# Optimization experiments

Hardware: AMD Instinct MI355X
Metric: run time of the kernel (lower is better)

The kernel has to match this reference:

```python
import jax, jax.numpy as jnp
import numpy as np
import math

B, T, D, H, P, NPASS = 2, 2048, 1024, 16, 256, 3


def setup_inputs() -> dict:
    key = jax.random.key(0)
    ks = jax.random.split(key, 8)
    x = jax.random.normal(ks[0], (B, T, D), jnp.float32)
    scale_gamma = 1.0 + 0.1 * jax.random.normal(ks[1], (D,), jnp.float32)
    scale_beta = 0.1 * jax.random.normal(ks[2], (D,), jnp.float32)
    qkv_w = 0.02 * jax.random.normal(ks[3], (3 * D, D), jnp.float32)
    o_w = 0.02 * jax.random.normal(ks[4], (D, D), jnp.float32)
    norm1_w = jnp.ones((D,), jnp.float32)
    norm2_w = jnp.ones((D,), jnp.float32)
    angles = 0.1 * jax.random.normal(ks[5], (NPASS, P), jnp.float32)
    gate = jnp.ones((NPASS, D), jnp.float32)
    bias = jnp.zeros((NPASS, D), jnp.float32)
    # seeded random permutations matching torch.manual_seed(42+p*1000); torch.randperm
    pis, pjs = [], []
    for p in range(NPASS):
        rng = np.random.RandomState(42 + p * 1000)
        perm = rng.permutation(D)
        pis.append(perm[:P])
        pjs.append(perm[P:2 * P])
    pi = jnp.asarray(np.stack(pis), jnp.int32)
    pj = jnp.asarray(np.stack(pjs), jnp.int32)
    return dict(x=x, scale_gamma=scale_gamma, scale_beta=scale_beta, qkv_w=qkv_w,
                o_w=o_w, norm1_w=norm1_w, norm2_w=norm2_w, angles=angles,
                gate=gate, bias=bias, pi=pi, pj=pj)


def _rmsnorm(x, w):
    eps = jnp.finfo(x.dtype).eps
    return x * jax.lax.rsqrt(jnp.mean(x * x, axis=-1, keepdims=True) + eps) * w


def reference(x, scale_gamma, scale_beta, qkv_w, o_w, norm1_w, norm2_w,
              angles, gate, bias, pi, pj):
    Bs, Ts, Ds = x.shape
    hd = Ds // H
    # --- attention branch ---
    h = _rmsnorm(x, norm1_w) * scale_gamma + scale_beta
    qkv = (h @ qkv_w.T).reshape(Bs, Ts, 3, H, hd)
    qkv = jnp.moveaxis(qkv, 2, 0)            # [3, B, T, H, hd]
    q, k, v = (jnp.swapaxes(qkv[i], 1, 2) for i in range(3))  # [B, H, T, hd]
    scores = jnp.einsum('bhqd,bhkd->bhqk', q, k) / math.sqrt(hd)
    causal = jnp.tril(jnp.ones((Ts, Ts), bool))
    scores = jnp.where(causal, scores, -jnp.inf)
    attn = jax.nn.softmax(scores, axis=-1)
    out = jnp.einsum('bhqk,bhkd->bhqd', attn, v)
    out = jnp.swapaxes(out, 1, 2).reshape(Bs, Ts, Ds)
    x = x + out @ o_w.T
    # --- rotation pseudo-FFN branch ---
    h = _rmsnorm(x, norm2_w) * scale_gamma + scale_beta
    r = h
    for p in range(NPASS):
        cos_a = jnp.cos(angles[p])
        sin_a = jnp.sin(angles[p])
        hi = r[..., pi[p]]
        hj = r[..., pj[p]]
        r = r.at[..., pi[p]].set(hi * cos_a - hj * sin_a)
        r = r.at[..., pj[p]].set(hi * sin_a + hj * cos_a)
        r = jax.nn.silu(r * gate[p] + bias[p])
    return x + r - h
```

## Files before the change

### kernel.cpp

```cpp
#include <hip/hip_runtime.h>
#include <hip/hip_bf16.h>

#define B_ 2
#define T_ 2048
#define D_ 1024
#define H_ 16
#define HD_ 64
#define NP_ 3
#define P_ 256

#define SCALE2 0.18033688011112042f

typedef short bf16x8 __attribute__((ext_vector_type(8)));
typedef float f32x4 __attribute__((ext_vector_type(4)));

__device__ __forceinline__ float bf2f(__hip_bfloat16 v) { return __bfloat162float(v); }
__device__ __forceinline__ __hip_bfloat16 f2bf(float v) { return __float2bfloat16(v); }

__device__ __forceinline__ unsigned pack2bf(float a, float b) {
    unsigned r;
    asm("v_cvt_pk_bf16_f32 %0, %1, %2" : "=v"(r) : "v"(a), "v"(b));
    return r;
}
__device__ __forceinline__ unsigned short f2bf_u(float v) {
    return (unsigned short)pack2bf(v, v);
}

#define GLOAD_LDS16(gp, lp) \
    __builtin_amdgcn_global_load_lds( \
        (const __attribute__((address_space(1))) void*)(gp), \
        (__attribute__((address_space(3))) void*)(lp), 16, 0, 0)

__global__ __launch_bounds__(256) void detect_kernel(
    const unsigned short* __restrict__ xs, int* __restrict__ flag)
{
    __shared__ int cnt;
    if (threadIdx.x == 0) cnt = 0;
    __syncthreads();
    int bad = 0;
    for (int i = threadIdx.x; i < 16384; i += 256) {
        int e = (xs[i] >> 7) & 0xFF;
        if (e >= 0xB8) bad++;
    }
    if (bad) atomicAdd(&cnt, bad);
    __syncthreads();
    if (threadIdx.x == 0) *flag = (cnt >= 8) ? 1 : 0;
}

__global__ __launch_bounds__(256) void prep_kernel(
    const void* __restrict__ xraw,
    const void* __restrict__ qkvw, const void* __restrict__ ow,
    const void* __restrict__ g,  const void* __restrict__ b,
    const void* __restrict__ n1, const void* __restrict__ n2,
    const void* __restrict__ ang, const void* __restrict__ gt,
    const void* __restrict__ bi,
    const int* __restrict__ flag,
    __hip_bfloat16* __restrict__ wbf, __hip_bfloat16* __restrict__ owbf,
    float* __restrict__ smalls, __hip_bfloat16* __restrict__ out)
{
    int bid = blockIdx.x;
    int t = threadIdx.x;
    int f = *flag;

    if (bid < 2048) {
        const int na = 3 * D_ * D_;
        int i8 = (bid * 256 + t) * 8;
        const void* src; __hip_bfloat16* dst; int off;
        if (i8 < na) { src = qkvw; dst = wbf; off = i8; }
        else         { src = ow;   dst = owbf; off = i8 - na; }
        if (f) {
            const float4* sp = (const float4*)((const float*)src + off);
            float4 v0 = sp[0], v1 = sp[1];
            uint4 o;
            o.x = pack2bf(v0.x, v0.y);
            o.y = pack2bf(v0.z, v0.w);
            o.z = pack2bf(v1.x, v1.y);
            o.w = pack2bf(v1.z, v1.w);
            *(uint4*)(dst + off) = o;
        } else {
            *(uint4*)(dst + off) = *(const uint4*)((const __hip_bfloat16*)src + off);
        }
        return;
    }
    if (bid < 6144) {
        int row = bid - 2048;
        float eps = f ? 1.1920929e-7f : 0.0078125f;
        float v[4], ga[4], be[4], ww[4];
        if (f) {
            const float4 xv = ((const float4*)((const float*)xraw + (size_t)row * D_))[t];
            v[0] = xv.x; v[1] = xv.y; v[2] = xv.z; v[3] = xv.w;
            const float4 gv = ((const float4*)g)[t];
            ga[0] = gv.x; ga[1] = gv.y; ga[2] = gv.z; ga[3] = gv.w;
            const float4 bv = ((const float4*)b)[t];
            be[0] = bv.x; be[1] = bv.y; be[2] = bv.z; be[3] = bv.w;
            const float4 wv4 = ((const float4*)n1)[t];
            ww[0] = wv4.x; ww[1] = wv4.y; ww[2] = wv4.z; ww[3] = wv4.w;
        } else {
            const uint2 u = ((const uint2*)((const __hip_bfloat16*)xraw + (size_t)row * D_))[t];
            v[0] = __uint_as_float(u.x << 16);
            v[1] = __uint_as_float(u.x & 0xffff0000u);
            v[2] = __uint_as_float(u.y << 16);
            v[3] = __uint_as_float(u.y & 0xffff0000u);
#pragma unroll
            for (int c = 0; c < 4; c++) {
                int e = t * 4 + c;
                ga[c] = bf2f(((const __hip_bfloat16*)g)[e]);
                be[c] = bf2f(((const __hip_bfloat16*)b)[e]);
                ww[c] = bf2f(((const __hip_bfloat16*)n1)[e]);
            }
        }
        float ss = 0.f;
#pragma unroll
        for (int c = 0; c < 4; c++) ss += v[c] * v[c];
#pragma unroll
        for (int m = 32; m; m >>= 1) ss += __shfl_xor(ss, m, 64);
        __shared__ float red[4];
        int wv = t >> 6;
        if ((t & 63) == 0) red[wv] = ss;
        __syncthreads();
        float scale = rsqrtf((red[0] + red[1] + red[2] + red[3]) * (1.0f / D_) + eps);
        float o[4];
#pragma unroll
        for (int c = 0; c < 4; c++)
            o[c] = v[c] * scale * ww[c] * ga[c] + be[c];
        uint2 pkd;
        pkd.x = pack2bf(o[0], o[1]);
        pkd.y = pack2bf(o[2], o[3]);
        *(uint2*)(out + (size_t)row * D_ + t * 4) = pkd;
        return;
    }
    {
        int i = (bid - 6144) * 256 + t;
        if (i >= 11008) return;
        const void* src; int off;
        if      (i < 1024) { src = g;   off = i; }
        else if (i < 2048) { src = b;   off = i - 1024; }
        else if (i < 3072) { src = n1;  off = i - 2048; }
        else if (i < 4096) { src = n2;  off = i - 3072; }
        else if (i < 4864) { src = ang; off = i - 4096; }
        else if (i < 7936) { src = gt;  off = i - 4864; }
        else               { src = bi;  off = i - 7936; }
        smalls[i] = f ? ((const float*)src)[off]
                      : bf2f(((const __hip_bfloat16*)src)[off]);
    }
}

__global__ __launch_bounds__(256) void gemm_bt_bf16_kernel(
    const __hip_bfloat16* __restrict__ A,
    const __hip_bfloat16* __restrict__ Bm,
    __hip_bfloat16* __restrict__ C,
    int M, int N, int K, int nscale, float qscale)
{
    __shared__ __attribute__((aligned(16))) __hip_bfloat16 As[128 * 32];
    __shared__ __attribute__((aligned(16))) __hip_bfloat16 Bs[128 * 32];
    int tid = threadIdx.x;
    int bm = blockIdx.y, bn = blockIdx.x;
    int lane = tid & 63, wv = tid >> 6;
    int wm = wv >> 1, wn = wv & 1;
    int q = lane >> 4, mr = lane & 15;

    f32x4 acc[4][4] = {};

    for (int k0 = 0; k0 < K; k0 += 32) {
#pragma unroll
        for (int s = 0; s < 2; s++) {
            int e = (s * 256 + tid) * 8;
            int r = e >> 5, c = e & 31;
            GLOAD_LDS16(&A[(size_t)(bm * 128 + r) * K + k0 + c], &As[e]);
            GLOAD_LDS16(&Bm[(size_t)(bn * 128 + r) * K + k0 + c], &Bs[e]);
        }
        __syncthreads();
        bf16x8 af[4], bfr[4];
#pragma unroll
        for (int i = 0; i < 4; i++)
            af[i] = *(const bf16x8*)(&As[(wm * 64 + i * 16 + mr) * 32 + q * 8]);
#pragma unroll
        for (int j = 0; j < 4; j++)
            bfr[j] = *(const bf16x8*)(&Bs[(wn * 64 + j * 16 + mr) * 32 + q * 8]);
#pragma unroll
        for (int i = 0; i < 4; i++)
#pragma unroll
            for (int j = 0; j < 4; j++)
                acc[i][j] = __builtin_amdgcn_mfma_f32_16x16x32_bf16(af[i], bfr[j], acc[i][j], 0, 0, 0);
        __syncthreads();
    }

#pragma unroll
    for (int i = 0; i < 4; i++)
#pragma unroll
        for (int r = 0; r < 4; r++) {
            int m = bm * 128 + wm * 64 + i * 16 + q * 4 + r;
#pragma unroll
            for (int j = 0; j < 4; j++) {
                int n = bn * 128 + wn * 64 + j * 16 + mr;
                float vv = acc[i][j][r];
                if (n < nscale) vv *= qscale;
                ((unsigned short*)C)[(size_t)m * N + n] = f2bf_u(vv);
            }
        }
}

__global__ __launch_bounds__(256) void gemm_o64_resid_kernel(
    const __hip_bfloat16* __restrict__ A,
    const __hip_bfloat16* __restrict__ Bm,
    const void* __restrict__ xraw,
    const int* __restrict__ flag,
    float* __restrict__ C,
    int M, int N, int K)
{
    __shared__ __attribute__((aligned(16))) __hip_bfloat16 As[128 * 32];
    __shared__ __attribute__((aligned(16))) __hip_bfloat16 Bs[64 * 32];
    int tid = threadIdx.x;
    int bn = blockIdx.x, bm = blockIdx.y;
    int lane = tid & 63, wv = tid >> 6;
    int q = lane >> 4, mr = lane & 15;
    int f = *flag;

    f32x4 acc[2][4] = {};

    for (int k0 = 0; k0 < K; k0 += 32) {
#pragma unroll
        for (int s = 0; s < 2; s++) {
            int e = (s * 256 + tid) * 8;
            int r = e >> 5, c = e & 31;
            GLOAD_LDS16(&A[(size_t)(bm * 128 + r) * K + k0 + c], &As[e]);
        }
        {
            int e = tid * 8;
            int r = e >> 5, c = e & 31;
            GLOAD_LDS16(&Bm[(size_t)(bn * 64 + r) * K + k0 + c], &Bs[e]);
        }
        __syncthreads();
        bf16x8 af[2], bfr[4];
#pragma unroll
        for (int i = 0; i < 2; i++)
            af[i] = *(const bf16x8*)(&As[(wv * 32 + i * 16 + mr) * 32 + q * 8]);
#pragma unroll
        for (int j = 0; j < 4; j++)
            bfr[j] = *(const bf16x8*)(&Bs[(j * 16 + mr) * 32 + q * 8]);
#pragma unroll
        for (int i = 0; i < 2; i++)
#pragma unroll
            for (int j = 0; j < 4; j++)
                acc[i][j] = __builtin_amdgcn_mfma_f32_16x16x32_bf16(af[i], bfr[j], acc[i][j], 0, 0, 0);
        __syncthreads();
    }

#pragma unroll
    for (int i = 0; i < 2; i++)
#pragma unroll
        for (int r = 0; r < 4; r++) {
            int m = bm * 128 + wv * 32 + i * 16 + q * 4 + r;
#pragma unroll
            for (int j = 0; j < 4; j++) {
                int n = bn * 64 + j * 16 + mr;
                size_t idx = (size_t)m * N + n;
                float rv = f ? ((const float*)xraw)[idx]
                             : bf2f(((const __hip_bfloat16*)xraw)[idx]);
                C[idx] = rv + acc[i][j][r];
            }
        }
}

__global__ __launch_bounds__(256, 4) void attn_kernel(
    const __hip_bfloat16* __restrict__ qkv,
    __hip_bfloat16* __restrict__ attn_out)
{
    __shared__ __attribute__((aligned(16))) __hip_bfloat16 Ks[2][64 * 64];
    __shared__ __attribute__((aligned(16))) __hip_bfloat16 Vts[2][64 * 64];
    __shared__ __attribute__((aligned(16))) unsigned int Pd[4 * 512];

    int id = blockIdx.x;
    int half = (id ^ (id >> 8)) & 1;
    int w4 = (id >> 1) & 15;
    int qt = half ? 31 - w4 : w4;
    int bh = (id >> 5) & 31;
    int b = bh >> 4, h = bh & 15;
    int tid = threadIdx.x, lane = tid & 63, wv = tid >> 6;
    int q = lane >> 4, mr = lane & 15;
    int m8 = mr & 7;

    const size_t rs3 = 3 * D_;
    const __hip_bfloat16* qp = qkv + (size_t)(b * T_) * rs3 + h * HD_;
    const __hip_bfloat16* kp = qp + D_;
    const __hip_bfloat16* vp = qp + 2 * D_;

    int sr = tid >> 2;
    int sc = (tid & 3) * 16;
    int lc0 = sc >> 3;
    int swk = sr & 7;
    int kk_ = (tid & 31) * 2;
    int dd = (tid >> 5) * 8;
    int vlc = kk_ >> 3, voff = kk_ & 7;

    bf16x8 aq0, aq1;
    {
        const __hip_bfloat16* qrow = qp + (size_t)(qt * 64 + wv * 16 + mr) * rs3;
        aq0 = *(const bf16x8*)(qrow + q * 8);
        aq1 = *(const bf16x8*)(qrow + 32 + q * 8);
    }

    bf16x8 kr0 = *(const bf16x8*)(kp + (size_t)sr * rs3 + sc);
    bf16x8 kr1 = *(const bf16x8*)(kp + (size_t)sr * rs3 + sc + 8);
    bf16x8 vr0 = *(const bf16x8*)(vp + (size_t)kk_ * rs3 + dd);
    bf16x8 vr1 = *(const bf16x8*)(vp + (size_t)(kk_ + 1) * rs3 + dd);
    *(bf16x8*)(&Ks[0][sr * 64 + ((lc0 ^ swk) * 8)]) = kr0;
    *(bf16x8*)(&Ks[0][sr * 64 + (((lc0 + 1) ^ swk) * 8)]) = kr1;
    {
        unsigned int* vd = (unsigned int*)&Vts[0][0];
        union { bf16x8 v; unsigned u[4]; } ua, ub;
        ua.v = vr0; ub.v = vr1;
#pragma unroll
        for (int w = 0; w < 4; w++) {
            unsigned lo = __builtin_amdgcn_perm(ub.u[w], ua.u[w], 0x05040100u);
            unsigned hi = __builtin_amdgcn_perm(ub.u[w], ua.u[w], 0x07060302u);
            int i0 = 2 * w, i1 = 2 * w + 1;
            vd[((dd + i0) * 64 + ((vlc ^ i0) * 8 + voff)) >> 1] = lo;
            vd[((dd + i1) * 64 + ((vlc ^ i1) * 8 + voff)) >> 1] = hi;
        }
    }
    __syncthreads();

    float l_part = 0.f;
    f32x4 o_acc[4] = {};
    unsigned int* Pw = &Pd[wv * 512];
    int qloc = wv * 16 + mr;

    for (int s = 0; s <= qt; s++) {
        int buf = s & 1;

        if (s < qt) {
            int ktn = s + 1;
            kr0 = *(const bf16x8*)(kp + (size_t)(ktn * 64 + sr) * rs3 + sc);
            kr1 = *(const bf16x8*)(kp + (size_t)(ktn * 64 + sr) * rs3 + sc + 8);
            vr0 = *(const bf16x8*)(vp + (size_t)(ktn * 64 + kk_) * rs3 + dd);
            vr1 = *(const bf16x8*)(vp + (size_t)(ktn * 64 + kk_ + 1) * rs3 + dd);
        }

        f32x4 sv[4] = {};
        {
            const __hip_bfloat16* Kb = &Ks[buf][0];
#pragma unroll
            for (int jn = 0; jn < 4; jn++)
                sv[jn] = __builtin_amdgcn_mfma_f32_16x16x32_bf16(
                    *(const bf16x8*)(&Kb[(jn * 16 + mr) * 64 + ((q ^ m8) * 8)]),
                    aq0, sv[jn], 0, 0, 0);
#pragma unroll
            for (int jn = 0; jn < 4; jn++)
                sv[jn] = __builtin_amdgcn_mfma_f32_16x16x32_bf16(
                    *(const bf16x8*)(&Kb[(jn * 16 + mr) * 64 + (((4 + q) ^ m8) * 8)]),
                    aq1, sv[jn], 0, 0, 0);
        }

        if (s == qt) {
#pragma unroll
            for (int jn = 0; jn < 4; jn++)
#pragma unroll
                for (int r = 0; r < 4; r++)
                    if (jn * 16 + q * 4 + r > qloc) sv[jn][r] = -1e30f;
        }

#pragma unroll
        for (int jn = 0; jn < 4; jn++)
#pragma unroll
            for (int r = 0; r < 4; r++) {
                float p = exp2f(sv[jn][r]);
                sv[jn][r] = p;
                l_part += p;
            }

#pragma unroll
        for (int jn = 0; jn < 4; jn++) {
            uint2 val;
            val.x = pack2bf(sv[jn][0], sv[jn][1]);
            val.y = pack2bf(sv[jn][2], sv[jn][3]);
            int dw4 = 2 * jn + (q >> 1);
            *(uint2*)(&Pw[mr * 32 + ((dw4 ^ m8) << 2) + 2 * (q & 1)]) = val;
        }

#pragma unroll
        for (int kk = 0; kk < 2; kk++) {
            bf16x8 bp = *(const bf16x8*)(&Pw[mr * 32 + (((4 * kk + q) ^ m8) << 2)]);
#pragma unroll
            for (int dt = 0; dt < 4; dt++) {
                bf16x8 bv = *(const bf16x8*)(&Vts[buf][(dt * 16 + mr) * 64 + (((kk * 4 + q) ^ m8) * 8)]);
                o_acc[dt] = __builtin_amdgcn_mfma_f32_16x16x32_bf16(bv, bp, o_acc[dt], 0, 0, 0);
            }
        }

        if (s < qt) {
            *(bf16x8*)(&Ks[buf ^ 1][sr * 64 + ((lc0 ^ swk) * 8)]) = kr0;
            *(bf16x8*)(&Ks[buf ^ 1][sr * 64 + (((lc0 + 1) ^ swk) * 8)]) = kr1;
            unsigned int* vd = (unsigned int*)&Vts[buf ^ 1][0];
            union { bf16x8 v; unsigned u[4]; } ua, ub;
            ua.v = vr0; ub.v = vr1;
#pragma unroll
            for (int w = 0; w < 4; w++) {
                unsigned lo = __builtin_amdgcn_perm(ub.u[w], ua.u[w], 0x05040100u);
                unsigned hi = __builtin_amdgcn_perm(ub.u[w], ua.u[w], 0x07060302u);
                int i0 = 2 * w, i1 = 2 * w + 1;
                vd[((dd + i0) * 64 + ((vlc ^ i0) * 8 + voff)) >> 1] = lo;
                vd[((dd + i1) * 64 + ((vlc ^ i1) * 8 + voff)) >> 1] = hi;
            }
        }
        __syncthreads();
    }

    float l_run = l_part;
    l_run += __shfl_xor(l_run, 16, 64);
    l_run += __shfl_xor(l_run, 32, 64);

    {
        float inv = 1.0f / l_run;
        int trow = qt * 64 + wv * 16 + mr;
        __hip_bfloat16* op = attn_out + (size_t)(b * T_ + trow) * D_ + h * HD_;
#pragma unroll
        for (int dt = 0; dt < 4; dt++) {
            uint2 val;
            val.x = pack2bf(o_acc[dt][0] * inv, o_acc[dt][1] * inv);
            val.y = pack2bf(o_acc[dt][2] * inv, o_acc[dt][3] * inv);
            *(uint2*)(op + dt * 16 + q * 4) = val;
        }
    }
}

__global__ __launch_bounds__(256) void final_kernel(
    const float* __restrict__ xn,
    const float* __restrict__ gamma,
    const float* __restrict__ beta,
    const float* __restrict__ w2,
    const float* __restrict__ angles,
    const float* __restrict__ gate,
    const float* __restrict__ bias,
    const int* __restrict__ pi,
    const int* __restrict__ pj,
    const int* __restrict__ flag,
    void* __restrict__ outp)
{
    __shared__ float rbuf[D_];
    __shared__ float red[4];
    int row = blockIdx.x, t = threadIdx.x;
    int f = *flag;
    float eps = f ? 1.1920929e-7f : 0.0078125f;
    const float4 xv = ((const float4*)(xn + (size_t)row * D_))[t];
    float x4[4] = {xv.x, xv.y, xv.z, xv.w};
    float ss = 0.f;
#pragma unroll
    for (int c = 0; c < 4; c++) ss += x4[c] * x4[c];
#pragma unroll
    for (int m = 32; m; m >>= 1) ss += __shfl_xor(ss, m, 64);
    int wv = t >> 6;
    if ((t & 63) == 0) red[wv] = ss;
    __syncthreads();
    float scale = rsqrtf((red[0] + red[1] + red[2] + red[3]) * (1.0f / D_) + eps);
    float hloc[4];
#pragma unroll
    for (int c = 0; c < 4; c++) {
        int e = t * 4 + c;
        float hv = x4[c] * scale * w2[e] * gamma[e] + beta[e];
        hloc[c] = hv;
        rbuf[e] = hv;
    }
    __syncthreads();
    for (int p = 0; p < NP_; p++) {
        float a = angles[p * P_ + t];
        float ca = __cosf(a), sa = __sinf(a);
        int ip = pi[p * P_ + t], jp = pj[p * P_ + t];
        float hi = rbuf[ip], hj = rbuf[jp];
        rbuf[ip] = hi * ca - hj * sa;
        rbuf[jp] = hi * sa + hj * ca;
        __syncthreads();
#pragma unroll
        for (int c = 0; c < 4; c++) {
            int e = t * 4 + c;
            float v = rbuf[e] * gate[p * D_ + e] + bias[p * D_ + e];
            rbuf[e] = v / (1.f + __expf(-v));
        }
        __syncthreads();
    }
#pragma unroll
    for (int c = 0; c < 4; c++) {
        int e = t * 4 + c;
        float ov = x4[c] + rbuf[e] - hloc[c];
        size_t idx = (size_t)row * D_ + e;
        if (f) ((float*)outp)[idx] = ov;
        else   ((__hip_bfloat16*)outp)[idx] = f2bf(ov);
    }
}

extern "C" void kernel_launch(void* const* d_in, const int* in_sizes, int n_in,
                              void* d_out, int out_size, void* d_ws, size_t ws_size,
                              hipStream_t stream)
{
    const void* x      = d_in[0];
    const void* gamma  = d_in[1];
    const void* beta   = d_in[2];
    const void* qkv_w  = d_in[3];
    const void* o_w    = d_in[4];
    const void* n1w    = d_in[5];
    const void* n2w    = d_in[6];
    const void* angles = d_in[7];
    const void* gate   = d_in[8];
    const void* bias   = d_in[9];
    const int* pi = (const int*)d_in[10];
    const int* pj = (const int*)d_in[11];

    const int M = B_ * T_;
    char* ws = (char*)d_ws;
    const size_t MB = 1u << 20;
    int*   flag   = (int*)ws;
    float* smalls = (float*)(ws + 4096);
    float* gf   = smalls;
    float* bf   = smalls + 1024;
    float* n2f  = smalls + 3072;
    float* angf = smalls + 4096;
    float* gtf  = smalls + 4864;
    float* bif  = smalls + 7936;
    __hip_bfloat16* wbf  = (__hip_bfloat16*)(ws + 17 * MB);
    __hip_bfloat16* owbf = (__hip_bfloat16*)(ws + 23 * MB);
    __hip_bfloat16* h1   = (__hip_bfloat16*)(ws + 25 * MB);
    __hip_bfloat16* qkv  = (__hip_bfloat16*)(ws + 33 * MB);
    float*          xnew = (float*)         (ws + 33 * MB);

    detect_kernel<<<1, 256, 0, stream>>>((const unsigned short*)x, flag);

    prep_kernel<<<6187, 256, 0, stream>>>(
        x, qkv_w, o_w, gamma, beta, n1w, n2w, angles, gate, bias,
        flag, wbf, owbf, smalls, h1);

    gemm_bt_bf16_kernel<<<dim3(3 * D_ / 128, M / 128), 256, 0, stream>>>(
        h1, wbf, qkv, M, 3 * D_, D_, D_, SCALE2);

    attn_kernel<<<dim3(1024), 256, 0, stream>>>(qkv, h1);

    gemm_o64_resid_kernel<<<dim3(D_ / 64, M / 128), 256, 0, stream>>>(
        h1, owbf, x, flag, xnew, M, D_, D_);

    final_kernel<<<M, 256, 0, stream>>>(xnew, gf, bf, n2f, angf, gtf, bif,
                                        pi, pj, flag, d_out);
}
```

Before: 235.1 us.

## Fuse dtype detection into prep, deepen GEMM K-tiles with swizzled LDS, prioritize MFMA

```diff
diff --git a/kernel.cpp b/kernel.cpp
--- a/kernel.cpp
+++ b/kernel.cpp
@@ -31,20 +31,22 @@
         (const __attribute__((address_space(1))) void*)(gp), \
         (__attribute__((address_space(3))) void*)(lp), 16, 0, 0)
 
-__global__ __launch_bounds__(256) void detect_kernel(
-    const unsigned short* __restrict__ xs, int* __restrict__ flag)
-{
-    __shared__ int cnt;
-    if (threadIdx.x == 0) cnt = 0;
+__device__ __forceinline__ int block_flag(const unsigned short* xs) {
+    __shared__ int fred[4];
+    int t = threadIdx.x;
+    uint4 v = ((const uint4*)xs)[t];
+    int bad = 0;
+    unsigned w[4] = {v.x, v.y, v.z, v.w};
+#pragma unroll
+    for (int i = 0; i < 4; i++) {
+        if ((((w[i] & 0xffffu) >> 7) & 0xFF) >= 0xB8) bad++;
+        if ((((w[i] >> 16)     >> 7) & 0xFF) >= 0xB8) bad++;
+    }
+#pragma unroll
+    for (int m = 32; m; m >>= 1) bad += __shfl_xor(bad, m, 64);
+    if ((t & 63) == 0) fred[t >> 6] = bad;
     __syncthreads();
-    int bad = 0;
-    for (int i = threadIdx.x; i < 16384; i += 256) {
-        int e = (xs[i] >> 7) & 0xFF;
-        if (e >= 0xB8) bad++;
-    }
-    if (bad) atomicAdd(&cnt, bad);
-    __syncthreads();
-    if (threadIdx.x == 0) *flag = (cnt >= 8) ? 1 : 0;
+    return (fred[0] + fred[1] + fred[2] + fred[3]) >= 8;
 }
 
 __global__ __launch_bounds__(256) void prep_kernel(
@@ -54,13 +56,14 @@
     const void* __restrict__ n1, const void* __restrict__ n2,
     const void* __restrict__ ang, const void* __restrict__ gt,
     const void* __restrict__ bi,
-    const int* __restrict__ flag,
+    int* __restrict__ flagp,
     __hip_bfloat16* __restrict__ wbf, __hip_bfloat16* __restrict__ owbf,
     float* __restrict__ smalls, __hip_bfloat16* __restrict__ out)
 {
     int bid = blockIdx.x;
     int t = threadIdx.x;
-    int f = *flag;
+    int f = block_flag((const unsigned short*)xraw);
+    if (bid == 0 && t == 0) *flagp = f;
 
     if (bid < 2048) {
         const int na = 3 * D_ * D_;
@@ -151,37 +154,43 @@
     __hip_bfloat16* __restrict__ C,
     int M, int N, int K, int nscale, float qscale)
 {
-    __shared__ __attribute__((aligned(16))) __hip_bfloat16 As[128 * 32];
-    __shared__ __attribute__((aligned(16))) __hip_bfloat16 Bs[128 * 32];
+    __shared__ __attribute__((aligned(16))) __hip_bfloat16 As[128 * 64];
+    __shared__ __attribute__((aligned(16))) __hip_bfloat16 Bs[128 * 64];
     int tid = threadIdx.x;
     int bm = blockIdx.y, bn = blockIdx.x;
     int lane = tid & 63, wv = tid >> 6;
     int wm = wv >> 1, wn = wv & 1;
     int q = lane >> 4, mr = lane & 15;
+    int m8 = mr & 7;
 
     f32x4 acc[4][4] = {};
 
-    for (int k0 = 0; k0 < K; k0 += 32) {
-#pragma unroll
-        for (int s = 0; s < 2; s++) {
+    for (int k0 = 0; k0 < K; k0 += 64) {
+#pragma unroll
+        for (int s = 0; s < 4; s++) {
             int e = (s * 256 + tid) * 8;
-            int r = e >> 5, c = e & 31;
-            GLOAD_LDS16(&A[(size_t)(bm * 128 + r) * K + k0 + c], &As[e]);
-            GLOAD_LDS16(&Bm[(size_t)(bn * 128 + r) * K + k0 + c], &Bs[e]);
-        }
-        __syncthreads();
-        bf16x8 af[4], bfr[4];
-#pragma unroll
-        for (int i = 0; i < 4; i++)
-            af[i] = *(const bf16x8*)(&As[(wm * 64 + i * 16 + mr) * 32 + q * 8]);
-#pragma unroll
-        for (int j = 0; j < 4; j++)
-            bfr[j] = *(const bf16x8*)(&Bs[(wn * 64 + j * 16 + mr) * 32 + q * 8]);
-#pragma unroll
-        for (int i = 0; i < 4; i++)
+            int r = e >> 6;
+            int pc = (e >> 3) & 7;
+            int gc = (pc ^ (r & 7)) * 8;
+            GLOAD_LDS16(&A[(size_t)(bm * 128 + r) * K + k0 + gc], &As[e]);
+            GLOAD_LDS16(&Bm[(size_t)(bn * 128 + r) * K + k0 + gc], &Bs[e]);
+        }
+        __syncthreads();
+#pragma unroll
+        for (int h = 0; h < 2; h++) {
+            bf16x8 af[4], bfr[4];
+#pragma unroll
+            for (int i = 0; i < 4; i++)
+                af[i] = *(const bf16x8*)(&As[(wm * 64 + i * 16 + mr) * 64 + (((h * 4 + q) ^ m8) * 8)]);
 #pragma unroll
             for (int j = 0; j < 4; j++)
-                acc[i][j] = __builtin_amdgcn_mfma_f32_16x16x32_bf16(af[i], bfr[j], acc[i][j], 0, 0, 0);
+                bfr[j] = *(const bf16x8*)(&Bs[(wn * 64 + j * 16 + mr) * 64 + (((h * 4 + q) ^ m8) * 8)]);
+#pragma unroll
+            for (int i = 0; i < 4; i++)
+#pragma unroll
+                for (int j = 0; j < 4; j++)
+                    acc[i][j] = __builtin_amdgcn_mfma_f32_16x16x32_bf16(af[i], bfr[j], acc[i][j], 0, 0, 0);
+        }
         __syncthreads();
     }
 
@@ -208,41 +217,50 @@
     float* __restrict__ C,
     int M, int N, int K)
 {
-    __shared__ __attribute__((aligned(16))) __hip_bfloat16 As[128 * 32];
-    __shared__ __attribute__((aligned(16))) __hip_bfloat16 Bs[64 * 32];
+    __shared__ __attribute__((aligned(16))) __hip_bfloat16 As[128 * 64];
+    __shared__ __attribute__((aligned(16))) __hip_bfloat16 Bs[64 * 64];
     int tid = threadIdx.x;
     int bn = blockIdx.x, bm = blockIdx.y;
     int lane = tid & 63, wv = tid >> 6;
     int q = lane >> 4, mr = lane & 15;
+    int m8 = mr & 7;
     int f = *flag;
 
     f32x4 acc[2][4] = {};
 
-    for (int k0 = 0; k0 < K; k0 += 32) {
+    for (int k0 = 0; k0 < K; k0 += 64) {
+#pragma unroll
+        for (int s = 0; s < 4; s++) {
+            int e = (s * 256 + tid) * 8;
+            int r = e >> 6;
+            int pc = (e >> 3) & 7;
+            int gc = (pc ^ (r & 7)) * 8;
+            GLOAD_LDS16(&A[(size_t)(bm * 128 + r) * K + k0 + gc], &As[e]);
+        }
 #pragma unroll
         for (int s = 0; s < 2; s++) {
             int e = (s * 256 + tid) * 8;
-            int r = e >> 5, c = e & 31;
-            GLOAD_LDS16(&A[(size_t)(bm * 128 + r) * K + k0 + c], &As[e]);
-        }
-        {
-            int e = tid * 8;
-            int r = e >> 5, c = e & 31;
-            GLOAD_LDS16(&Bm[(size_t)(bn * 64 + r) * K + k0 + c], &Bs[e]);
-        }
-        __syncthreads();
-        bf16x8 af[2], bfr[4];
-#pragma unroll
-        for (int i = 0; i < 2; i++)
-            af[i] = *(const bf16x8*)(&As[(wv * 32 + i * 16 + mr) * 32 + q * 8]);
-#pragma unroll
-        for (int j = 0; j < 4; j++)
-            bfr[j] = *(const bf16x8*)(&Bs[(j * 16 + mr) * 32 + q * 8]);
-#pragma unroll
-        for (int i = 0; i < 2; i++)
+            int r = e >> 6;
+            int pc = (e >> 3) & 7;
+            int gc = (pc ^ (r & 7)) * 8;
+            GLOAD_LDS16(&Bm[(size_t)(bn * 64 + r) * K + k0 + gc], &Bs[e]);
+        }
+        __syncthreads();
+#pragma unroll
+        for (int h = 0; h < 2; h++) {
+            bf16x8 af[2], bfr[4];
+#pragma unroll
+            for (int i = 0; i < 2; i++)
+                af[i] = *(const bf16x8*)(&As[(wv * 32 + i * 16 + mr) * 64 + (((h * 4 + q) ^ m8) * 8)]);
 #pragma unroll
             for (int j = 0; j < 4; j++)
-                acc[i][j] = __builtin_amdgcn_mfma_f32_16x16x32_bf16(af[i], bfr[j], acc[i][j], 0, 0, 0);
+                bfr[j] = *(const bf16x8*)(&Bs[(j * 16 + mr) * 64 + (((h * 4 + q) ^ m8) * 8)]);
+#pragma unroll
+            for (int i = 0; i < 2; i++)
+#pragma unroll
+                for (int j = 0; j < 4; j++)
+                    acc[i][j] = __builtin_amdgcn_mfma_f32_16x16x32_bf16(af[i], bfr[j], acc[i][j], 0, 0, 0);
+        }
         __syncthreads();
     }
 
@@ -340,6 +358,7 @@
         f32x4 sv[4] = {};
         {
             const __hip_bfloat16* Kb = &Ks[buf][0];
+            __builtin_amdgcn_s_setprio(1);
 #pragma unroll
             for (int jn = 0; jn < 4; jn++)
                 sv[jn] = __builtin_amdgcn_mfma_f32_16x16x32_bf16(
@@ -350,6 +369,7 @@
                 sv[jn] = __builtin_amdgcn_mfma_f32_16x16x32_bf16(
                     *(const bf16x8*)(&Kb[(jn * 16 + mr) * 64 + (((4 + q) ^ m8) * 8)]),
                     aq1, sv[jn], 0, 0, 0);
+            __builtin_amdgcn_s_setprio(0);
         }
 
         if (s == qt) {
@@ -378,6 +398,7 @@
             *(uint2*)(&Pw[mr * 32 + ((dw4 ^ m8) << 2) + 2 * (q & 1)]) = val;
         }
 
+        __builtin_amdgcn_s_setprio(1);
 #pragma unroll
         for (int kk = 0; kk < 2; kk++) {
             bf16x8 bp = *(const bf16x8*)(&Pw[mr * 32 + (((4 * kk + q) ^ m8) << 2)]);
@@ -387,6 +408,7 @@
                 o_acc[dt] = __builtin_amdgcn_mfma_f32_16x16x32_bf16(bv, bp, o_acc[dt], 0, 0, 0);
             }
         }
+        __builtin_amdgcn_s_setprio(0);
 
         if (s < qt) {
             *(bf16x8*)(&Ks[buf ^ 1][sr * 64 + ((lc0 ^ swk) * 8)]) = kr0;
@@ -522,8 +544,6 @@
     __hip_bfloat16* qkv  = (__hip_bfloat16*)(ws + 33 * MB);
     float*          xnew = (float*)         (ws + 33 * MB);
 
-    detect_kernel<<<1, 256, 0, stream>>>((const unsigned short*)x, flag);
-
     prep_kernel<<<6187, 256, 0, stream>>>(
         x, qkv_w, o_w, gamma, beta, n1w, n2w, angles, gate, bias,
         flag, wbf, owbf, smalls, h1);
```

Result: faster. 213.6 us, median of 2 (-9.1%).
